# Kernel optimization log

Measured on AMD Instinct MI355X. Metric: run time of the kernel, lower is better.

The kernel has to match this reference:

```python
import jax, jax.numpy as jnp
import numpy as np

N = 20000   # nodes
E = 320000  # edges (avg degree 16)
IN = 16     # in_node_nf
H = 64      # hidden_nf
OUT = 64    # out_node_nf
L = 4       # n_layers


def setup_inputs() -> dict:
    key = jax.random.key(0)
    ks = jax.random.split(key, 16)
    w = lambda k, shape: (jax.random.normal(k, shape, dtype=jnp.float32) * 0.05)
    zb = lambda *shape: jnp.zeros(shape, dtype=jnp.float32)
    return {
        "h": jax.random.normal(ks[0], (N, IN), dtype=jnp.float32),
        "x": jax.random.normal(ks[1], (N, 3), dtype=jnp.float32),
        "edge_index": jax.random.randint(ks[2], (2, E), 0, N),
        "emb_in_w": w(ks[3], (IN, H)), "emb_in_b": zb(H),
        "edge_w1": w(ks[4], (L, 2 * H + 1, H)), "edge_b1": zb(L, H),
        "edge_w2": w(ks[5], (L, H, H)), "edge_b2": zb(L, H),
        "coord_w1": w(ks[6], (L, H, H)), "coord_b1": zb(L, H),
        "coord_w2": w(ks[7], (L, H, 1)),  # bias-free last coord_mlp layer
        "node_w1": w(ks[8], (L, 2 * H, H)), "node_b1": zb(L, H),
        "node_w2": w(ks[9], (L, H, H)), "node_b2": zb(L, H),
        "emb_out_w": w(ks[10], (H, OUT)), "emb_out_b": zb(OUT),
    }


def reference(h, x, edge_index, emb_in_w, emb_in_b,
              edge_w1, edge_b1, edge_w2, edge_b2,
              coord_w1, coord_b1, coord_w2,
              node_w1, node_b1, node_w2, node_b2,
              emb_out_w, emb_out_b):
    row, col = edge_index[0], edge_index[1]
    act = jax.nn.silu
    # receiver in-degree for mean coordinate aggregation (clamped to >=1)
    cnt = jax.ops.segment_sum(jnp.ones((row.shape[0], 1), h.dtype), row, num_segments=N)
    cnt = jnp.maximum(cnt, 1.0)

    h = h @ emb_in_w + emb_in_b
    for l in range(L):
        # coord2radial
        diff = x[row] - x[col]                               # [E,3]
        radial = jnp.sum(diff * diff, axis=-1, keepdims=True)  # [E,1]
        # edge model: m_ij = phi_e(h_i, h_j, ||x_i-x_j||^2)
        e_in = jnp.concatenate([h[row], h[col], radial], axis=-1)  # [E,2H+1]
        m = act(e_in @ edge_w1[l] + edge_b1[l])
        m = act(m @ edge_w2[l] + edge_b2[l])                 # [E,H]
        # coord model: x_i += mean_j (x_i - x_j) * phi_x(m_ij)
        phi = act(m @ coord_w1[l] + coord_b1[l]) @ coord_w2[l]  # [E,1]
        trans = diff * phi                                    # [E,3]
        x = x + jax.ops.segment_sum(trans, row, num_segments=N) / cnt
        # node model: h_i = h_i + phi_h(h_i, sum_j m_ij)
        agg = jax.ops.segment_sum(m, row, num_segments=N)     # [N,H]
        n_in = jnp.concatenate([h, agg], axis=-1)             # [N,2H]
        out = act(n_in @ node_w1[l] + node_b1[l]) @ node_w2[l] + node_b2[l]
        h = h + out
    h = h @ emb_out_w + emb_out_b
    return h, x
```

## Files before the change

kernel.cpp:

```cpp
#include <hip/hip_runtime.h>
#include <hip/hip_bf16.h>


#define NN 20000
#define EE 320000
#define LSE 17024
#define LSN 6272

typedef unsigned short u16;
typedef unsigned int   u32;
typedef __attribute__((ext_vector_type(8))) short s16x8;
typedef __attribute__((ext_vector_type(4))) float f32x4;

__device__ __forceinline__ float bf2f(u16 u) { return __uint_as_float(((u32)u) << 16); }
__device__ __forceinline__ float silu_f(float x) { return x / (1.0f + __expf(-x)); }

__device__ __forceinline__ u16 f2bf_rne(float f) {
    u32 u = __float_as_uint(f);
    return (u16)((u + 0x7FFFu + ((u >> 16) & 1u)) >> 16);
}
__device__ __forceinline__ float gldf(const void* p, int i, int bf) {
    return bf ? bf2f(((const u16*)p)[i]) : ((const float*)p)[i];
}
__device__ __forceinline__ u16 gldb(const void* p, int i, int bf) {
    return bf ? ((const u16*)p)[i] : f2bf_rne(((const float*)p)[i]);
}

__global__ void k_detect(const u16* __restrict__ h_raw, int* __restrict__ flag) {
    __shared__ int cnt_s;
    int tid = threadIdx.x;
    if (tid == 0) cnt_s = 0;
    __syncthreads();
    float v = fabsf(bf2f(h_raw[tid]));
    int ok = (v >= 0.015625f && v <= 16.0f) ? 1 : 0;
    atomicAdd(&cnt_s, ok);
    __syncthreads();
    if (tid == 0) *flag = (cnt_s >= 96) ? 1 : 0;
}

__global__ void k_sentinel(u16* __restrict__ out, int n, float v) {
    int t = blockIdx.x * 256 + threadIdx.x;
    if (t < n) out[t] = f2bf_rne(v);
}

__global__ __launch_bounds__(256) void k_pack(
    const void* __restrict__ ew1, const void* __restrict__ eb1,
    const void* __restrict__ ew2, const void* __restrict__ eb2,
    const void* __restrict__ cw1, const void* __restrict__ cb1,
    const void* __restrict__ cw2,
    const void* __restrict__ nw1, const void* __restrict__ nb1,
    const void* __restrict__ nw2, const void* __restrict__ nb2,
    const int* __restrict__ flag, u16* __restrict__ pkE, u32* __restrict__ pkN)
{
    const int bf = *flag;
    const int gid = blockIdx.x * 256 + threadIdx.x;
    const int stride = gridDim.x * 256;

    for (int g = gid; g < 4 * 16384; g += stride) {
        int l = g >> 14, idx = g & 16383;
        u16 v;
        if (idx < 8192) {
            int j = idx & 7, lane = (idx >> 3) & 63, t = (idx >> 9) & 3, w = idx >> 11;
            int k = 32 * w + (lane >> 4) * 8 + j, n = 16 * t + (lane & 15);
            v = gldb(ew1, l * 129 * 64 + k * 64 + n, bf);
        } else if (idx < 12288) {
            int i2 = idx - 8192;
            int j = i2 & 7, lane = (i2 >> 3) & 63, t = (i2 >> 9) & 3, w = i2 >> 11;
            int k = 32 * w + (lane >> 4) * 8 + j, n = 16 * t + (lane & 15);
            v = gldb(ew2, l * 4096 + k * 64 + n, bf);
        } else {
            int i2 = idx - 12288;
            int j = i2 & 7, lane = (i2 >> 3) & 63, t = (i2 >> 9) & 3, w = i2 >> 11;
            int k = 32 * w + (lane >> 4) * 8 + j, n = 16 * t + (lane & 15);
            v = gldb(cw1, l * 4096 + k * 64 + n, bf);
        }
        pkE[l * LSE + idx] = v;
    }
    for (int g = gid; g < 4 * 320; g += stride) {
        int l = g / 320, r = g % 320, wch = r >> 6, i = r & 63;
        float v = (wch == 0) ? gldf(eb1, l * 64 + i, bf)
                : (wch == 1) ? gldf(eb2, l * 64 + i, bf)
                : (wch == 2) ? gldf(cb1, l * 64 + i, bf)
                : (wch == 3) ? gldf(cw2, l * 64 + i, bf)
                :              gldf(ew1, l * 129 * 64 + 128 * 64 + i, bf);
        ((float*)(pkE + l * LSE + 16384))[r] = v;
    }
    for (int g = gid; g < 4 * 6144; g += stride) {
        int l = g / 6144, idx = g % 6144;
        u32 pv;
        if (idx < 4096) {
            int kp = idx >> 6, j = idx & 63;
            u32 lo = gldb(nw1, l * 8192 + (2 * kp) * 64 + j, bf);
            u32 hi = gldb(nw1, l * 8192 + (2 * kp + 1) * 64 + j, bf);
            pv = lo | (hi << 16);
        } else {
            int i2 = idx - 4096, kp = i2 >> 6, j = i2 & 63;
            u32 lo = gldb(nw2, l * 4096 + (2 * kp) * 64 + j, bf);
            u32 hi = gldb(nw2, l * 4096 + (2 * kp + 1) * 64 + j, bf);
            pv = lo | (hi << 16);
        }
        pkN[l * LSN + idx] = pv;
    }
    for (int g = gid; g < 4 * 128; g += stride) {
        int l = g >> 7, r = g & 127;
        float v = (r < 64) ? gldf(nb1, l * 64 + r, bf) : gldf(nb2, l * 64 + (r - 64), bf);
        ((float*)(pkN + l * LSN + 6144))[r] = v;
    }
}

__global__ void k_deg(const int* __restrict__ rowi, int* __restrict__ deg) {
    int e = blockIdx.x * 256 + threadIdx.x;
    if (e < EE) atomicAdd(&deg[rowi[e]], 1);
}

__global__ __launch_bounds__(1024) void k_scan(const int* deg, int* offs, int* cursor) {
    __shared__ int part[1024];
    const int tid = threadIdx.x;
    const int CH = (NN + 1023) / 1024;
    const int b0 = tid * CH;
    int s = 0;
    for (int i = 0; i < CH; i++) { int idx = b0 + i; if (idx < NN) s += deg[idx]; }
    part[tid] = s;
    __syncthreads();
    for (int d = 1; d < 1024; d <<= 1) {
        int v = (tid >= d) ? part[tid - d] : 0;
        __syncthreads();
        part[tid] += v;
        __syncthreads();
    }
    int run = (tid > 0) ? part[tid - 1] : 0;
    for (int i = 0; i < CH; i++) {
        int idx = b0 + i;
        if (idx < NN) {
            int dv = deg[idx];
            offs[idx] = run;
            cursor[idx] = run;
            run += dv;
        }
    }
    if (tid == 1023) offs[NN] = run;
}

__global__ void k_scatter(const int* __restrict__ rowi, const int* __restrict__ coli,
                          int* __restrict__ cursor, int* __restrict__ slist) {
    int e = blockIdx.x * 256 + threadIdx.x;
    if (e < EE) {
        int r = rowi[e];
        int pos = atomicAdd(&cursor[r], 1);
        slist[pos] = coli[e];
    }
}

__global__ __launch_bounds__(256) void k_embed(
    const void* __restrict__ h_in, const void* __restrict__ x_in,
    const void* __restrict__ w, const void* __restrict__ bias,
    const int* __restrict__ flag,
    float* __restrict__ hws, float* __restrict__ xws, u16* __restrict__ hb)
{
    const int bf = *flag;
    const int lane = threadIdx.x & 63;
    const int wv   = threadIdx.x >> 6;
    const int i    = blockIdx.x * 4 + wv;
    float acc = gldf(bias, lane, bf);
    #pragma unroll
    for (int k = 0; k < 16; k++)
        acc = fmaf(gldf(h_in, i * 16 + k, bf), gldf(w, k * 64 + lane, bf), acc);
    hws[i * 64 + lane] = acc;
    hb[i * 64 + lane] = f2bf_rne(acc);
    if (lane < 3) xws[i * 3 + lane] = gldf(x_in, i * 3 + lane, bf);
}

#define OFF_B23  8192
#define OFF_M    16384
#define MPAD     76
#define OFF_PHI  (OFF_M + 4 * 16 * MPAD)
__global__ __launch_bounds__(256, 3) void k_edge(
    const u16* __restrict__ hb, const float* __restrict__ xws,
    const int* __restrict__ offs, const int* __restrict__ slist,
    const u16* __restrict__ pE,
    float* __restrict__ agg, float* __restrict__ xacc)
{
    __shared__ __align__(16) u16 sW[OFF_PHI + 4 * 16 * 2];

    const int tid = threadIdx.x, lane = tid & 63, wv = tid >> 6;
    const int l15 = lane & 15, quad = lane >> 4;

    for (int idx = tid; idx < 2048; idx += 256)
        ((s16x8*)sW)[idx] = ((const s16x8*)pE)[idx];
    const float* pb = (const float*)(pE + 16384);
    float b1v[4], b2v[4], cb1v[4], c2v[4], wrv[4];
    #pragma unroll
    for (int t = 0; t < 4; t++) {
        b1v[t]  = pb[       16 * t + l15];
        b2v[t]  = pb[ 64 +  16 * t + l15];
        cb1v[t] = pb[128 +  16 * t + l15];
        c2v[t]  = pb[192 +  16 * t + l15];
        wrv[t]  = pb[256 +  16 * t + l15];
    }
    __syncthreads();

    const int gw = blockIdx.x * 4 + wv, totW = gridDim.x * 4;
    u16* mrow = &sW[OFF_M + wv * 16 * MPAD];
    float* phiw = (float*)&sW[OFF_PHI + wv * 32];

    for (int n = gw; n < NN; n += totW) {
        const int o0 = offs[n], deg = offs[n + 1] - o0;
        if (deg == 0) continue;

        const s16x8 Ar0 = *(const s16x8*)&hb[n * 64 + quad * 8];
        const s16x8 Ar1 = *(const s16x8*)&hb[n * 64 + 32 + quad * 8];
        const float xrv = (quad < 3) ? xws[n * 3 + quad] : 0.0f;
        float aggA[4] = {0.f, 0.f, 0.f, 0.f};
        float xaccA = 0.0f;

        for (int eb = 0; eb < deg; eb += 16) {
            const int nb = min(16, deg - eb);
            const int ee = (l15 < nb) ? l15 : 0;
            const int ce = slist[o0 + eb + ee];
            float dx = 0.0f;
            if (quad < 3 && l15 < nb) dx = xrv - xws[ce * 3 + quad];
            float r2 = dx * dx;
            r2 += __shfl_xor(r2, 16, 64);
            r2 += __shfl_xor(r2, 32, 64);

            f32x4 C[4] = {{0,0,0,0},{0,0,0,0},{0,0,0,0},{0,0,0,0}};
            #pragma unroll
            for (int t = 0; t < 4; t++) {
                const s16x8 Bf0 = *(const s16x8*)&sW[((0 * 4 + t) * 64 + lane) * 8];
                C[t] = __builtin_amdgcn_mfma_f32_16x16x32_bf16(Ar0, Bf0, C[t], 0, 0, 0);
                const s16x8 Bf1 = *(const s16x8*)&sW[((1 * 4 + t) * 64 + lane) * 8];
                C[t] = __builtin_amdgcn_mfma_f32_16x16x32_bf16(Ar1, Bf1, C[t], 0, 0, 0);
            }
            {
                const s16x8 Ac0 = *(const s16x8*)&hb[ce * 64 + quad * 8];
                const s16x8 Ac1 = *(const s16x8*)&hb[ce * 64 + 32 + quad * 8];
                #pragma unroll
                for (int t = 0; t < 4; t++) {
                    const s16x8 Bf2 = *(const s16x8*)&sW[((2 * 4 + t) * 64 + lane) * 8];
                    C[t] = __builtin_amdgcn_mfma_f32_16x16x32_bf16(Ac0, Bf2, C[t], 0, 0, 0);
                    const s16x8 Bf3 = *(const s16x8*)&sW[((3 * 4 + t) * 64 + lane) * 8];
                    C[t] = __builtin_amdgcn_mfma_f32_16x16x32_bf16(Ac1, Bf3, C[t], 0, 0, 0);
                }
            }
            float r2r[4];
            #pragma unroll
            for (int r = 0; r < 4; r++) r2r[r] = __shfl(r2, quad * 4 + r, 64);
            #pragma unroll
            for (int t = 0; t < 4; t++)
                #pragma unroll
                for (int r = 0; r < 4; r++) {
                    float v = silu_f(C[t][r] + b1v[t] + r2r[r] * wrv[t]);
                    mrow[(quad * 4 + r) * MPAD + 16 * t + l15] = f2bf_rne(v);
                }

            f32x4 D[4] = {{0,0,0,0},{0,0,0,0},{0,0,0,0},{0,0,0,0}};
            #pragma unroll
            for (int w = 0; w < 2; w++) {
                const s16x8 Am = *(const s16x8*)(mrow + l15 * MPAD + 32 * w + quad * 8);
                #pragma unroll
                for (int t = 0; t < 4; t++) {
                    const s16x8 Bf = *(const s16x8*)&sW[OFF_B23 + ((w * 4 + t) * 64 + lane) * 8];
                    D[t] = __builtin_amdgcn_mfma_f32_16x16x32_bf16(Am, Bf, D[t], 0, 0, 0);
                }
            }
            #pragma unroll
            for (int t = 0; t < 4; t++)
                #pragma unroll
                for (int r = 0; r < 4; r++) {
                    float v = silu_f(D[t][r] + b2v[t]);
                    if (quad * 4 + r < nb) aggA[t] += v;
                    mrow[(quad * 4 + r) * MPAD + 16 * t + l15] = f2bf_rne(v);
                }

            f32x4 P[4] = {{0,0,0,0},{0,0,0,0},{0,0,0,0},{0,0,0,0}};
            #pragma unroll
            for (int w = 0; w < 2; w++) {
                const s16x8 Am = *(const s16x8*)(mrow + l15 * MPAD + 32 * w + quad * 8);
                #pragma unroll
                for (int t = 0; t < 4; t++) {
                    const s16x8 Bf = *(const s16x8*)&sW[OFF_B23 + (((2 + w) * 4 + t) * 64 + lane) * 8];
                    P[t] = __builtin_amdgcn_mfma_f32_16x16x32_bf16(Am, Bf, P[t], 0, 0, 0);
                }
            }
            float ph[4];
            #pragma unroll
            for (int r = 0; r < 4; r++) {
                float s = 0.f;
                #pragma unroll
                for (int t = 0; t < 4; t++) s = fmaf(silu_f(P[t][r] + cb1v[t]), c2v[t], s);
                s += __shfl_xor(s, 1, 64);
                s += __shfl_xor(s, 2, 64);
                s += __shfl_xor(s, 4, 64);
                s += __shfl_xor(s, 8, 64);
                ph[r] = s;
            }
            if (l15 == 0) {
                #pragma unroll
                for (int r = 0; r < 4; r++) phiw[quad * 4 + r] = ph[r];
            }
            float phv = phiw[l15];
            if (quad < 3 && l15 < nb) xaccA = fmaf(dx, phv, xaccA);
        }

        #pragma unroll
        for (int t = 0; t < 4; t++) {
            aggA[t] += __shfl_xor(aggA[t], 16, 64);
            aggA[t] += __shfl_xor(aggA[t], 32, 64);
        }
        float av = (quad == 0) ? aggA[0] : (quad == 1) ? aggA[1]
                 : (quad == 2) ? aggA[2] : aggA[3];
        agg[n * 64 + quad * 16 + l15] = av;

        xaccA += __shfl_xor(xaccA, 1, 64);
        xaccA += __shfl_xor(xaccA, 2, 64);
        xaccA += __shfl_xor(xaccA, 4, 64);
        xaccA += __shfl_xor(xaccA, 8, 64);
        if (l15 == 0 && quad < 3) xacc[n * 3 + quad] = xaccA / (float)deg;
    }
}

__global__ void k_coord(float* __restrict__ xws, const float* __restrict__ xacc) {
    int t = blockIdx.x * 256 + threadIdx.x;
    if (t < NN * 3) xws[t] += xacc[t];
}

__global__ __launch_bounds__(256) void k_node(
    float* __restrict__ hws, u16* __restrict__ hb, const float* __restrict__ agg,
    const u32* __restrict__ pN)
{
    __shared__ __align__(16) u32 sW1p[64 * 64];
    __shared__ __align__(16) u32 sW2p[32 * 64];
    __shared__ float sB1f[64], sB2f[64];
    __shared__ __align__(16) float sNin[4][8][132];

    const int tid = threadIdx.x, lane = tid & 63, wv = tid >> 6;
    for (int idx = tid; idx < 1024; idx += 256)
        ((f32x4*)sW1p)[idx] = ((const f32x4*)pN)[idx];
    for (int idx = tid; idx < 512; idx += 256)
        ((f32x4*)sW2p)[idx] = ((const f32x4*)(pN + 4096))[idx];
    const float* pb = (const float*)(pN + 6144);
    if (tid < 64) { sB1f[tid] = pb[tid]; sB2f[tid] = pb[64 + tid]; }
    __syncthreads();

    const int i0 = (blockIdx.x * 4 + wv) * 8;
    float hold[8];
    #pragma unroll
    for (int b = 0; b < 8; b++) {
        int i = i0 + b;
        float hv = hws[i * 64 + lane];
        hold[b] = hv;
        sNin[wv][b][lane]      = hv;
        sNin[wv][b][64 + lane] = agg[i * 64 + lane];
    }

    float acc[8];
    #pragma unroll
    for (int b = 0; b < 8; b++) acc[b] = sB1f[lane];
    #pragma unroll
    for (int kk = 0; kk < 32; kk++) {
        u32 w01 = sW1p[(kk * 2) * 64 + lane];
        u32 w23 = sW1p[(kk * 2 + 1) * 64 + lane];
        float w0 = __uint_as_float(w01 << 16), w1 = __uint_as_float(w01 & 0xffff0000u);
        float w2 = __uint_as_float(w23 << 16), w3 = __uint_as_float(w23 & 0xffff0000u);
        #pragma unroll
        for (int b = 0; b < 8; b++) {
            const float4 e4 = *reinterpret_cast<const float4*>(&sNin[wv][b][kk * 4]);
            acc[b] = fmaf(e4.x, w0, fmaf(e4.y, w1, fmaf(e4.z, w2, fmaf(e4.w, w3, acc[b]))));
        }
    }
    #pragma unroll
    for (int b = 0; b < 8; b++) acc[b] = silu_f(acc[b]);
    #pragma unroll
    for (int b = 0; b < 8; b++) sNin[wv][b][lane] = acc[b];

    float out[8];
    #pragma unroll
    for (int b = 0; b < 8; b++) out[b] = sB2f[lane];
    #pragma unroll
    for (int kk = 0; kk < 16; kk++) {
        u32 w01 = sW2p[(kk * 2) * 64 + lane];
        u32 w23 = sW2p[(kk * 2 + 1) * 64 + lane];
        float w0 = __uint_as_float(w01 << 16), w1 = __uint_as_float(w01 & 0xffff0000u);
        float w2 = __uint_as_float(w23 << 16), w3 = __uint_as_float(w23 & 0xffff0000u);
        #pragma unroll
        for (int b = 0; b < 8; b++) {
            const float4 e4 = *reinterpret_cast<const float4*>(&sNin[wv][b][kk * 4]);
            out[b] = fmaf(e4.x, w0, fmaf(e4.y, w1, fmaf(e4.z, w2, fmaf(e4.w, w3, out[b]))));
        }
    }
    #pragma unroll
    for (int b = 0; b < 8; b++) {
        float hv = hold[b] + out[b];
        hws[(i0 + b) * 64 + lane] = hv;
        hb[(i0 + b) * 64 + lane] = f2bf_rne(hv);
    }
}

__global__ __launch_bounds__(256) void k_out(
    const float* __restrict__ hws, const float* __restrict__ xws,
    const void* __restrict__ wo, const void* __restrict__ bo,
    const int* __restrict__ flag, void* __restrict__ out)
{
    __shared__ u32 sWp[32 * 64];
    __shared__ float sBf[64];
    __shared__ __align__(16) float sH[4][8][68];
    const int tid = threadIdx.x, lane = tid & 63, wv = tid >> 6;
    const int bf = *flag;
    for (int idx = tid; idx < 32 * 64; idx += 256) {
        int kp = idx >> 6, j = idx & 63;
        u32 lo = gldb(wo, (kp * 2) * 64 + j, bf);
        u32 hi = gldb(wo, (kp * 2 + 1) * 64 + j, bf);
        sWp[idx] = lo | (hi << 16);
    }
    if (tid < 64) sBf[tid] = gldf(bo, tid, bf);
    __syncthreads();

    const int i0 = (blockIdx.x * 4 + wv) * 8;
    #pragma unroll
    for (int b = 0; b < 8; b++) sH[wv][b][lane] = hws[(i0 + b) * 64 + lane];

    float acc[8];
    #pragma unroll
    for (int b = 0; b < 8; b++) acc[b] = sBf[lane];
    #pragma unroll
    for (int kk = 0; kk < 16; kk++) {
        u32 w01 = sWp[(kk * 2) * 64 + lane];
        u32 w23 = sWp[(kk * 2 + 1) * 64 + lane];
        float w0 = __uint_as_float(w01 << 16), w1 = __uint_as_float(w01 & 0xffff0000u);
        float w2 = __uint_as_float(w23 << 16), w3 = __uint_as_float(w23 & 0xffff0000u);
        #pragma unroll
        for (int b = 0; b < 8; b++) {
            const float4 e4 = *reinterpret_cast<const float4*>(&sH[wv][b][kk * 4]);
            acc[b] = fmaf(e4.x, w0, fmaf(e4.y, w1, fmaf(e4.z, w2, fmaf(e4.w, w3, acc[b]))));
        }
    }
    u16*   oh16 = (u16*)out;
    float* ohf  = (float*)out;
    u16*   ox16 = oh16 + (size_t)NN * 64;
    float* oxf  = ohf  + (size_t)NN * 64;
    #pragma unroll
    for (int b = 0; b < 8; b++) {
        int i = i0 + b;
        if (bf) {
            oh16[i * 64 + lane] = f2bf_rne(acc[b]);
            if (lane < 3) ox16[i * 3 + lane] = f2bf_rne(xws[i * 3 + lane]);
        } else {
            ohf[i * 64 + lane] = acc[b];
            if (lane < 3) oxf[i * 3 + lane] = xws[i * 3 + lane];
        }
    }
}

extern "C" void kernel_launch(void* const* d_in, const int* in_sizes, int n_in,
                              void* d_out, int out_size, void* d_ws, size_t ws_size,
                              hipStream_t stream)
{
    const size_t WS_REQ = (size_t)NN * 134 * sizeof(float) + 64;
    if (ws_size < WS_REQ) {
        float sval = 1000.0f + (float)(ws_size >> 20);
        k_sentinel<<<(out_size + 255) / 256, 256, 0, stream>>>(
            (u16*)d_out, out_size, sval);
        return;
    }

    const void* h_in = d_in[0];
    const void* x_in = d_in[1];
    const int*  eidx = (const int*)d_in[2];
    const int* rowi = eidx;
    const int* coli = eidx + EE;

    float* ws   = (float*)d_ws;
    float* hws  = ws;
    float* xws  = hws + NN * 64;
    float* agg  = xws + NN * 3;
    float* xacc = agg + NN * 64;
    int*   flag = (int*)(xacc + NN * 3);
    int*   cursor = (int*)xacc;

    u16* hb    = (u16*)d_out;
    int* offs  = (int*)(hb + (size_t)NN * 64);
    int* slist = offs + (NN + 4);
    u16* pkE   = (u16*)(slist + EE);
    u32* pkN   = (u32*)(pkE + 4 * LSE);

    hipMemsetAsync(cursor, 0, (size_t)NN * sizeof(int), stream);

    k_detect<<<1, 128, 0, stream>>>((const u16*)h_in, flag);
    k_pack<<<64, 256, 0, stream>>>(d_in[5], d_in[6], d_in[7], d_in[8], d_in[9],
                                   d_in[10], d_in[11], d_in[12], d_in[13],
                                   d_in[14], d_in[15], flag, pkE, pkN);
    k_deg<<<(EE + 255) / 256, 256, 0, stream>>>(rowi, cursor);
    k_scan<<<1, 1024, 0, stream>>>(cursor, offs, cursor);
    k_scatter<<<(EE + 255) / 256, 256, 0, stream>>>(rowi, coli, cursor, slist);

    hipMemsetAsync(agg, 0, (size_t)NN * 67 * sizeof(float), stream);

    k_embed<<<NN / 4, 256, 0, stream>>>(h_in, x_in, d_in[3], d_in[4], flag, hws, xws, hb);

    for (int l = 0; l < 4; l++) {
        k_edge<<<1536, 256, 0, stream>>>(hb, xws, offs, slist,
                                         pkE + l * LSE, agg, xacc);
        k_coord<<<(NN * 3 + 255) / 256, 256, 0, stream>>>(xws, xacc);
        k_node<<<NN / 32, 256, 0, stream>>>(hws, hb, agg, pkN + (size_t)l * LSN);
    }
    k_out<<<NN / 32, 256, 0, stream>>>(hws, xws, d_in[16], d_in[17], flag, d_out);
}
```

Measured before the change: 593.5 us.

## Fuse setup kernels, hoist receiver GEMM out of edge loop, merge coord update

Merges dtype detection and degree counting into the weight-packing kernel, and folds the coordinate update into the node kernel, so fewer kernels are launched. In the edge kernel, the receiver-half MFMA products are computed once per node instead of once per 16-edge batch. The edge grid is halved to 768 blocks and the cursor buffer moves to a separate region. Each block re-runs the detection reduction, and the coord update inside k_node depends on the node grid covering exactly NN*3 entries.

```diff
diff --git a/kernel.cpp b/kernel.cpp
--- a/kernel.cpp
+++ b/kernel.cpp
@@ -24,18 +24,6 @@
 }
 __device__ __forceinline__ u16 gldb(const void* p, int i, int bf) {
     return bf ? ((const u16*)p)[i] : f2bf_rne(((const float*)p)[i]);
-}
-
-__global__ void k_detect(const u16* __restrict__ h_raw, int* __restrict__ flag) {
-    __shared__ int cnt_s;
-    int tid = threadIdx.x;
-    if (tid == 0) cnt_s = 0;
-    __syncthreads();
-    float v = fabsf(bf2f(h_raw[tid]));
-    int ok = (v >= 0.015625f && v <= 16.0f) ? 1 : 0;
-    atomicAdd(&cnt_s, ok);
-    __syncthreads();
-    if (tid == 0) *flag = (cnt_s >= 96) ? 1 : 0;
 }
 
 __global__ void k_sentinel(u16* __restrict__ out, int n, float v) {
@@ -50,11 +38,28 @@
     const void* __restrict__ cw2,
     const void* __restrict__ nw1, const void* __restrict__ nb1,
     const void* __restrict__ nw2, const void* __restrict__ nb2,
-    const int* __restrict__ flag, u16* __restrict__ pkE, u32* __restrict__ pkN)
+    const u16* __restrict__ h_raw, const int* __restrict__ rowi,
+    int* __restrict__ flag, int* __restrict__ deg,
+    u16* __restrict__ pkE, u32* __restrict__ pkN)
 {
-    const int bf = *flag;
+    if (blockIdx.x >= 64) {
+        int e = (blockIdx.x - 64) * 256 + threadIdx.x;
+        if (e < EE) atomicAdd(&deg[rowi[e]], 1);
+        return;
+    }
+    __shared__ int cnt_s;
+    if (threadIdx.x == 0) cnt_s = 0;
+    __syncthreads();
+    if (threadIdx.x < 128) {
+        float v = fabsf(bf2f(h_raw[threadIdx.x]));
+        if (v >= 0.015625f && v <= 16.0f) atomicAdd(&cnt_s, 1);
+    }
+    __syncthreads();
+    const int bf = (cnt_s >= 96) ? 1 : 0;
+    if (blockIdx.x == 0 && threadIdx.x == 0) *flag = bf;
+
     const int gid = blockIdx.x * 256 + threadIdx.x;
-    const int stride = gridDim.x * 256;
+    const int stride = 64 * 256;
 
     for (int g = gid; g < 4 * 16384; g += stride) {
         int l = g >> 14, idx = g & 16383;
@@ -108,11 +113,6 @@
     }
 }
 
-__global__ void k_deg(const int* __restrict__ rowi, int* __restrict__ deg) {
-    int e = blockIdx.x * 256 + threadIdx.x;
-    if (e < EE) atomicAdd(&deg[rowi[e]], 1);
-}
-
 __global__ __launch_bounds__(1024) void k_scan(const int* deg, int* offs, int* cursor) {
     __shared__ int part[1024];
     const int tid = threadIdx.x;
@@ -209,6 +209,14 @@
 
         const s16x8 Ar0 = *(const s16x8*)&hb[n * 64 + quad * 8];
         const s16x8 Ar1 = *(const s16x8*)&hb[n * 64 + 32 + quad * 8];
+        f32x4 Cb[4] = {{0,0,0,0},{0,0,0,0},{0,0,0,0},{0,0,0,0}};
+        #pragma unroll
+        for (int t = 0; t < 4; t++) {
+            const s16x8 Bf0 = *(const s16x8*)&sW[((0 * 4 + t) * 64 + lane) * 8];
+            Cb[t] = __builtin_amdgcn_mfma_f32_16x16x32_bf16(Ar0, Bf0, Cb[t], 0, 0, 0);
+            const s16x8 Bf1 = *(const s16x8*)&sW[((1 * 4 + t) * 64 + lane) * 8];
+            Cb[t] = __builtin_amdgcn_mfma_f32_16x16x32_bf16(Ar1, Bf1, Cb[t], 0, 0, 0);
+        }
         const float xrv = (quad < 3) ? xws[n * 3 + quad] : 0.0f;
         float aggA[4] = {0.f, 0.f, 0.f, 0.f};
         float xaccA = 0.0f;
@@ -223,14 +231,7 @@
             r2 += __shfl_xor(r2, 16, 64);
             r2 += __shfl_xor(r2, 32, 64);
 
-            f32x4 C[4] = {{0,0,0,0},{0,0,0,0},{0,0,0,0},{0,0,0,0}};
-            #pragma unroll
-            for (int t = 0; t < 4; t++) {
-                const s16x8 Bf0 = *(const s16x8*)&sW[((0 * 4 + t) * 64 + lane) * 8];
-                C[t] = __builtin_amdgcn_mfma_f32_16x16x32_bf16(Ar0, Bf0, C[t], 0, 0, 0);
-                const s16x8 Bf1 = *(const s16x8*)&sW[((1 * 4 + t) * 64 + lane) * 8];
-                C[t] = __builtin_amdgcn_mfma_f32_16x16x32_bf16(Ar1, Bf1, C[t], 0, 0, 0);
-            }
+            f32x4 C[4] = {Cb[0], Cb[1], Cb[2], Cb[3]};
             {
                 const s16x8 Ac0 = *(const s16x8*)&hb[ce * 64 + quad * 8];
                 const s16x8 Ac1 = *(const s16x8*)&hb[ce * 64 + 32 + quad * 8];
@@ -319,13 +320,9 @@
     }
 }
 
-__global__ void k_coord(float* __restrict__ xws, const float* __restrict__ xacc) {
-    int t = blockIdx.x * 256 + threadIdx.x;
-    if (t < NN * 3) xws[t] += xacc[t];
-}
-
 __global__ __launch_bounds__(256) void k_node(
     float* __restrict__ hws, u16* __restrict__ hb, const float* __restrict__ agg,
+    float* __restrict__ xws, const float* __restrict__ xacc,
     const u32* __restrict__ pN)
 {
     __shared__ __align__(16) u32 sW1p[64 * 64];
@@ -340,6 +337,11 @@
         ((f32x4*)sW2p)[idx] = ((const f32x4*)(pN + 4096))[idx];
     const float* pb = (const float*)(pN + 6144);
     if (tid < 64) { sB1f[tid] = pb[tid]; sB2f[tid] = pb[64 + tid]; }
+
+    {
+        int t = blockIdx.x * 96 + tid;
+        if (tid < 96) xws[t] += xacc[t];
+    }
     __syncthreads();
 
     const int i0 = (blockIdx.x * 4 + wv) * 8;
@@ -475,33 +477,30 @@
     float* agg  = xws + NN * 3;
     float* xacc = agg + NN * 64;
     int*   flag = (int*)(xacc + NN * 3);
-    int*   cursor = (int*)xacc;
-
-    u16* hb    = (u16*)d_out;
-    int* offs  = (int*)(hb + (size_t)NN * 64);
-    int* slist = offs + (NN + 4);
-    u16* pkE   = (u16*)(slist + EE);
-    u32* pkN   = (u32*)(pkE + 4 * LSE);
+
+    u16* hb     = (u16*)d_out;
+    int* offs   = (int*)(hb + (size_t)NN * 64);
+    int* slist  = offs + (NN + 4);
+    u16* pkE    = (u16*)(slist + EE);
+    u32* pkN    = (u32*)(pkE + 4 * LSE);
+    int* cursor = (int*)(pkN + 4 * LSN);
 
     hipMemsetAsync(cursor, 0, (size_t)NN * sizeof(int), stream);
-
-    k_detect<<<1, 128, 0, stream>>>((const u16*)h_in, flag);
-    k_pack<<<64, 256, 0, stream>>>(d_in[5], d_in[6], d_in[7], d_in[8], d_in[9],
-                                   d_in[10], d_in[11], d_in[12], d_in[13],
-                                   d_in[14], d_in[15], flag, pkE, pkN);
-    k_deg<<<(EE + 255) / 256, 256, 0, stream>>>(rowi, cursor);
+    hipMemsetAsync(agg, 0, (size_t)NN * 67 * sizeof(float), stream);
+
+    k_pack<<<64 + (EE + 255) / 256, 256, 0, stream>>>(
+        d_in[5], d_in[6], d_in[7], d_in[8], d_in[9], d_in[10], d_in[11],
+        d_in[12], d_in[13], d_in[14], d_in[15],
+        (const u16*)h_in, rowi, flag, cursor, pkE, pkN);
     k_scan<<<1, 1024, 0, stream>>>(cursor, offs, cursor);
     k_scatter<<<(EE + 255) / 256, 256, 0, stream>>>(rowi, coli, cursor, slist);
-
-    hipMemsetAsync(agg, 0, (size_t)NN * 67 * sizeof(float), stream);
-
     k_embed<<<NN / 4, 256, 0, stream>>>(h_in, x_in, d_in[3], d_in[4], flag, hws, xws, hb);
 
     for (int l = 0; l < 4; l++) {
-        k_edge<<<1536, 256, 0, stream>>>(hb, xws, offs, slist,
-                                         pkE + l * LSE, agg, xacc);
-        k_coord<<<(NN * 3 + 255) / 256, 256, 0, stream>>>(xws, xacc);
-        k_node<<<NN / 32, 256, 0, stream>>>(hws, hb, agg, pkN + (size_t)l * LSN);
+        k_edge<<<768, 256, 0, stream>>>(hb, xws, offs, slist,
+                                        pkE + l * LSE, agg, xacc);
+        k_node<<<NN / 32, 256, 0, stream>>>(hws, hb, agg, xws, xacc,
+                                            pkN + (size_t)l * LSN);
     }
     k_out<<<NN / 32, 256, 0, stream>>>(hws, xws, d_in[16], d_in[17], flag, d_out);
 }
```

Result: faster. 581.0 us (median of 2 runs) (-2.1%).
